# Optimization experiments

Measured on AMD Instinct MI355X. Metric: run time of the kernel, lower is better.

The kernel has to match this reference:

```python
import jax, jax.numpy as jnp
import numpy as np

B = 32768
IN_DIM, OUT_DIM, VAR_DIM = 2, 3, 50
KER_DIMS = [1024, 1024, 1024, 1024]
NSTEPS = 32  # fixed-step RK4 stand-in for adaptive odeint over t in [0, 1]


def setup_inputs() -> dict:
    key = jax.random.key(0)
    ks = jax.random.split(key, 11)
    x = jax.random.normal(ks[0], (B, IN_DIM), dtype=jnp.float32)
    dims = [VAR_DIM] + KER_DIMS + [VAR_DIM]
    inp = {"x": x}
    for i, (d1, d2) in enumerate(zip(dims[:-1], dims[1:])):
        # torch Linear(d1+1, d2): weight (d2, d1+1); stored here as (d1+1, d2)
        bound = 1.0 / np.sqrt(d1 + 1)
        inp[f"W{i}"] = jax.random.uniform(ks[1 + 2 * i], (d1 + 1, d2), jnp.float32, -bound, bound)
        inp[f"b{i}"] = jax.random.uniform(ks[2 + 2 * i], (d2,), jnp.float32, -bound, bound)
    return inp


def _odefunc(t, y, Ws, bs):
    # Each layer: concat time column, Linear, ReLU (except last) -- matches ODEfunc.forward
    out = y
    n = len(Ws)
    for i in range(n):
        tcol = jnp.full((out.shape[0], 1), t, dtype=out.dtype)
        h = jnp.concatenate([out, tcol], axis=1)
        out = h @ Ws[i] + bs[i]
        if i < n - 1:
            out = jax.nn.relu(out)
    return out


def _integrate(x, Ws, bs):
    # Pad input into var_dim state: out[:, :in_dim] = x, rest zeros
    y0 = jnp.zeros((x.shape[0], VAR_DIM), dtype=x.dtype).at[:, : x.shape[1]].set(x)
    dt = jnp.asarray(1.0 / NSTEPS, dtype=x.dtype)
    ts = jnp.arange(NSTEPS, dtype=x.dtype) * dt

    def step(y, t):
        k1 = _odefunc(t, y, Ws, bs)
        k2 = _odefunc(t + dt * 0.5, y + dt * 0.5 * k1, Ws, bs)
        k3 = _odefunc(t + dt * 0.5, y + dt * 0.5 * k2, Ws, bs)
        k4 = _odefunc(t + dt, y + dt * k3, Ws, bs)
        return y + (dt / 6.0) * (k1 + 2.0 * k2 + 2.0 * k3 + k4), None

    y1, _ = jax.lax.scan(step, y0, ts)
    return y1[:, :OUT_DIM]


def reference(x, W0, b0, W1, b1, W2, b2, W3, b3, W4, b4):
    Ws = (W0, W1, W2, W3, W4)
    bs = (b0, b1, b2, b3, b4)
    return _integrate(x, Ws, bs)
```

## Files before the change

kernel.cpp:

```cpp
#include <hip/hip_runtime.h>
#include <hip/hip_bf16.h>
#include <stdint.h>


typedef __bf16 bf16_t;
typedef bf16_t bf16x8 __attribute__((ext_vector_type(8)));
typedef float  f32x4  __attribute__((ext_vector_type(4)));

#define DEVI static __device__ __forceinline__

DEVI void gload_lds16(const bf16_t* gsrc, bf16_t* ldst) {
  __builtin_amdgcn_global_load_lds(
      (const __attribute__((address_space(1))) uint32_t*)gsrc,
      (__attribute__((address_space(3))) uint32_t*)ldst,
      16, 0, 0);
}

template<int K>
__global__ __launch_bounds__(512, 2) void gemm256(
    const bf16_t* __restrict__ A,
    const bf16_t* __restrict__ BT,
    const float* __restrict__ bias,
    const float* __restrict__ wtime,
    float t,
    bf16_t* __restrict__ C, int ldc,
    int M, int N)
{
  constexpr int NT = K / 64;
  static_assert(NT >= 2, "need >=2 K-tiles");

  __shared__ __align__(16) bf16_t As[2][256][64];
  __shared__ __align__(16) bf16_t Bs[2][256][64];

  const int tid  = threadIdx.x;
  const int wave = tid >> 6;
  const int lane = tid & 63;
  const int wr = wave >> 2;
  const int wc = wave & 3;

  int wg = blockIdx.x;
  {
    const int cpx = gridDim.x >> 3;
    wg = (wg & 7) * cpx + (wg >> 3);
  }
  const int nbn = N >> 8;
  const int bm = (wg / nbn) << 8;
  const int bn = (wg % nbn) << 8;

  const int srow = lane >> 3;
  const int scol = ((lane & 7) << 3) ^ ((lane & 32) >> 1) ^ ((wave & 1) << 5);
  const bf16_t* aS = A  + (size_t)(bm + wave * 8 + srow) * K + scol;
  const bf16_t* bS = BT + (size_t)(bn + wave * 8 + srow) * K + scol;
  bf16_t* aD = &As[0][0][0] + wave * 8 * 64;
  bf16_t* bD = &Bs[0][0][0] + wave * 8 * 64;

  auto stageHalf = [&](int kt, int isB, int h) {
    const int buf = kt & 1;
    const bf16_t* src = (isB ? bS : aS) + (size_t)(h * 128) * K + kt * 64;
    bf16_t*       dst = (isB ? bD : aD) + (buf * 256 + h * 128) * 64;
    gload_lds16(src,                 dst);
    gload_lds16(src + (size_t)64 * K, dst + 64 * 64);
  };

  const int fr = lane & 15;
  const int fq = lane >> 4;
  const int rsw = ((fr & 4) << 3) ^ ((fr & 8) << 3);

  bf16x8 af[8];
  bf16x8 bfr[8];
  f32x4  acc[8][4] = {};

  auto lda_frag = [&](int buf, int mh) {
    const char* base = (const char*)&As[buf][0][0];
#pragma unroll
    for (int m = 0; m < 4; ++m)
#pragma unroll
      for (int kk = 0; kk < 2; ++kk) {
        int r  = wr * 128 + (mh * 4 + m) * 16 + fr;
        int cb = (kk * 64 + fq * 16) ^ rsw;
        af[m * 2 + kk] = *(const bf16x8*)(base + r * 128 + cb);
      }
  };
  auto ldb_frag = [&](int buf, int nh) {
    const char* base = (const char*)&Bs[buf][0][0];
#pragma unroll
    for (int n = 0; n < 2; ++n)
#pragma unroll
      for (int kk = 0; kk < 2; ++kk) {
        int r  = wc * 64 + (nh * 2 + n) * 16 + fr;
        int cb = (kk * 64 + fq * 16) ^ rsw;
        bfr[nh * 4 + n * 2 + kk] = *(const bf16x8*)(base + r * 128 + cb);
      }
  };
  auto mma_quad = [&](int mh, int nh) {
    __builtin_amdgcn_s_setprio(1);
#pragma unroll
    for (int m = 0; m < 4; ++m)
#pragma unroll
      for (int n = 0; n < 2; ++n)
#pragma unroll
        for (int kk = 0; kk < 2; ++kk)
          acc[mh * 4 + m][nh * 2 + n] = __builtin_amdgcn_mfma_f32_16x16x32_bf16(
              af[m * 2 + kk], bfr[nh * 4 + n * 2 + kk],
              acc[mh * 4 + m][nh * 2 + n], 0, 0, 0);
    __builtin_amdgcn_s_setprio(0);
  };

  stageHalf(0, 0, 0); stageHalf(0, 1, 0);
  stageHalf(0, 0, 1); stageHalf(0, 1, 1);
  stageHalf(1, 1, 0); stageHalf(1, 0, 0);
  asm volatile("s_waitcnt vmcnt(4)" ::: "memory");
  __builtin_amdgcn_s_barrier();

  for (int t2 = 0; t2 < NT; ++t2) {
    const int buf = t2 & 1;
    lda_frag(buf, 0);
    ldb_frag(buf, 0);
    if (t2 + 1 < NT) stageHalf(t2 + 1, 0, 1);
    __builtin_amdgcn_s_barrier();
    mma_quad(0, 0);
    __builtin_amdgcn_s_barrier();
    ldb_frag(buf, 1);
    if (t2 + 1 < NT) stageHalf(t2 + 1, 1, 1);
    __builtin_amdgcn_s_barrier();
    mma_quad(0, 1);
    __builtin_amdgcn_s_barrier();
    lda_frag(buf, 1);
    if (t2 + 2 < NT) stageHalf(t2 + 2, 1, 0);
    __builtin_amdgcn_s_barrier();
    mma_quad(1, 0);
    __builtin_amdgcn_s_barrier();
    if (t2 + 2 < NT) {
      stageHalf(t2 + 2, 0, 0);
      asm volatile("s_waitcnt vmcnt(4)" ::: "memory");
    } else {
      asm volatile("s_waitcnt vmcnt(0)" ::: "memory");
    }
    __builtin_amdgcn_s_barrier();
    mma_quad(1, 1);
    __builtin_amdgcn_s_barrier();
  }

#pragma unroll
  for (int n = 0; n < 4; ++n) {
    const int gcol = bn + wc * 64 + n * 16 + fr;
    const float bv = bias[gcol] + t * wtime[gcol];
#pragma unroll
    for (int m = 0; m < 8; ++m) {
      const int grow0 = bm + wr * 128 + m * 16 + (fq << 2);
#pragma unroll
      for (int r = 0; r < 4; ++r) {
        float v = acc[m][n][r] + bv;
        v = v > 0.0f ? v : 0.0f;
        C[(size_t)(grow0 + r) * ldc + gcol] = (bf16_t)v;
      }
    }
  }
}

template<int BM, int BN, int BK, int WROWS, int WCOLS, bool RELU, bool OUT_BF16>
__global__ __launch_bounds__(256) void gemm_bt(
    const bf16_t* __restrict__ A, int lda,
    const bf16_t* __restrict__ BT,
    const float* __restrict__ bias,
    const float* __restrict__ wtime,
    float t,
    void* __restrict__ Cv, int ldc,
    int M, int K)
{
  static_assert(BK == 64, "swizzle assumes BK=64");
  constexpr int MR  = BM / WROWS / 16;
  constexpr int NR  = BN / WCOLS / 16;
  constexpr int TPR = BK / 8;
  constexpr int RPW = 64 / TPR;
  constexpr int RPL = 4 * RPW;
  static_assert(BM % RPL == 0 && BN % RPL == 0, "tile staging mismatch");

  __shared__ bf16_t As[BM][BK];
  __shared__ bf16_t Bs[BN][BK];

  const int tid  = threadIdx.x;
  const int wave = tid >> 6;
  const int lane = tid & 63;
  const int wr = wave / WCOLS;
  const int wc = wave % WCOLS;
  const int bm = blockIdx.x * BM;
  const int bn = blockIdx.y * BN;
  const int lrow = lane >> 3;
  const int lcol = (((lane & 7) << 3) ^ ((lane & 32) >> 1) ^ ((wave & 1) << 5));

  const int fr = lane & 15;
  const int fq = lane >> 4;
  const int esw = ((fr & 4) << 2) ^ ((fr & 8) << 2);

  f32x4 acc[MR][NR] = {};

  for (int k0 = 0; k0 < K; k0 += BK) {
#pragma unroll
    for (int i = 0; i < BM / RPL; ++i) {
      const int rb = i * RPL + wave * RPW;
      gload_lds16(&A[(size_t)(bm + rb + lrow) * lda + k0 + lcol], &As[rb][0]);
    }
#pragma unroll
    for (int i = 0; i < BN / RPL; ++i) {
      const int rb = i * RPL + wave * RPW;
      gload_lds16(&BT[(size_t)(bn + rb + lrow) * K + k0 + lcol], &Bs[rb][0]);
    }
    __syncthreads();
#pragma unroll
    for (int kk = 0; kk < BK / 32; ++kk) {
      bf16x8 af[MR], bfr[NR];
      const int ecol = (kk * 32 + fq * 8) ^ esw;
#pragma unroll
      for (int m = 0; m < MR; ++m)
        af[m] = *(const bf16x8*)&As[wr * (BM / WROWS) + m * 16 + fr][ecol];
#pragma unroll
      for (int n = 0; n < NR; ++n)
        bfr[n] = *(const bf16x8*)&Bs[wc * (BN / WCOLS) + n * 16 + fr][ecol];
#pragma unroll
      for (int m = 0; m < MR; ++m)
#pragma unroll
        for (int n = 0; n < NR; ++n)
          acc[m][n] = __builtin_amdgcn_mfma_f32_16x16x32_bf16(
              af[m], bfr[n], acc[m][n], 0, 0, 0);
    }
    __syncthreads();
  }

#pragma unroll
  for (int n = 0; n < NR; ++n) {
    const int gcol = bn + wc * (BN / WCOLS) + n * 16 + fr;
    const float bv = bias[gcol] + t * wtime[gcol];
#pragma unroll
    for (int m = 0; m < MR; ++m) {
      const int grow0 = bm + wr * (BM / WROWS) + m * 16 + (fq << 2);
#pragma unroll
      for (int r = 0; r < 4; ++r) {
        float v = acc[m][n][r] + bv;
        if (RELU) v = v > 0.0f ? v : 0.0f;
        if constexpr (OUT_BF16)
          ((bf16_t*)Cv)[(size_t)(grow0 + r) * ldc + gcol] = (bf16_t)v;
        else
          ((float*)Cv)[(size_t)(grow0 + r) * ldc + gcol] = v;
      }
    }
  }
}

__global__ __launch_bounds__(256) void gemm_l4_rk4(
    const bf16_t* __restrict__ A, int lda,
    const bf16_t* __restrict__ BT,
    const float* __restrict__ bias,
    const float* __restrict__ wtime,
    float t,
    float* __restrict__ y, float* __restrict__ accb,
    bf16_t* __restrict__ ybf,
    float ca, float cs, int mode,
    int M, int K)
{
  constexpr int BM = 64, BN = 64, BK = 64;
  constexpr int MR = 2, NR = 2;

  __shared__ bf16_t As[BM][BK];
  __shared__ bf16_t Bs[BN][BK];

  const int tid  = threadIdx.x;
  const int wave = tid >> 6;
  const int lane = tid & 63;
  const int wr = wave >> 1;
  const int wc = wave & 1;
  const int bm = blockIdx.x * BM;
  const int lrow = lane >> 3;
  const int lcol = (((lane & 7) << 3) ^ ((lane & 32) >> 1) ^ ((wave & 1) << 5));

  const int fr = lane & 15;
  const int fq = lane >> 4;
  const int esw = ((fr & 4) << 2) ^ ((fr & 8) << 2);

  f32x4 acc[MR][NR] = {};

  for (int k0 = 0; k0 < K; k0 += BK) {
#pragma unroll
    for (int i = 0; i < 2; ++i) {
      const int rb = i * 32 + wave * 8;
      gload_lds16(&A[(size_t)(bm + rb + lrow) * lda + k0 + lcol], &As[rb][0]);
    }
#pragma unroll
    for (int i = 0; i < 2; ++i) {
      const int rb = i * 32 + wave * 8;
      gload_lds16(&BT[(size_t)(rb + lrow) * K + k0 + lcol], &Bs[rb][0]);
    }
    __syncthreads();
#pragma unroll
    for (int kk = 0; kk < 2; ++kk) {
      bf16x8 af[MR], bfr[NR];
      const int ecol = (kk * 32 + fq * 8) ^ esw;
#pragma unroll
      for (int m = 0; m < MR; ++m)
        af[m] = *(const bf16x8*)&As[wr * 32 + m * 16 + fr][ecol];
#pragma unroll
      for (int n = 0; n < NR; ++n)
        bfr[n] = *(const bf16x8*)&Bs[wc * 32 + n * 16 + fr][ecol];
#pragma unroll
      for (int m = 0; m < MR; ++m)
#pragma unroll
        for (int n = 0; n < NR; ++n)
          acc[m][n] = __builtin_amdgcn_mfma_f32_16x16x32_bf16(
              af[m], bfr[n], acc[m][n], 0, 0, 0);
    }
    __syncthreads();
  }

#pragma unroll
  for (int n = 0; n < NR; ++n) {
    const int gcol = wc * 32 + n * 16 + fr;
    const float bv = bias[gcol] + t * wtime[gcol];
#pragma unroll
    for (int m = 0; m < MR; ++m) {
      const int grow0 = bm + wr * 32 + m * 16 + (fq << 2);
#pragma unroll
      for (int r = 0; r < 4; ++r) {
        const float kv = acc[m][n][r] + bv;
        const size_t o = (size_t)(grow0 + r) * 64 + gcol;
        if (mode == 0) {
          accb[o] = kv;
          ybf[o] = (bf16_t)(y[o] + cs * kv);
        } else if (mode == 1) {
          accb[o] += ca * kv;
          ybf[o] = (bf16_t)(y[o] + cs * kv);
        } else {
          const float ny = y[o] + cs * (accb[o] + kv);
          y[o] = ny;
          ybf[o] = (bf16_t)ny;
        }
      }
    }
  }
}

__global__ void prep_weight(const float* __restrict__ W, const float* __restrict__ b,
                            bf16_t* __restrict__ WT, float* __restrict__ bias,
                            float* __restrict__ wtime,
                            int K, int N, int Kpad, int Npad)
{
  int idx = blockIdx.x * 256 + threadIdx.x;
  int total = Npad * Kpad;
  if (idx < total) {
    int n = idx / Kpad, k = idx % Kpad;
    float v = (n < N && k < K) ? W[(size_t)k * N + n] : 0.0f;
    WT[idx] = (bf16_t)v;
  }
  if (idx < Npad) {
    bias[idx]  = (idx < N) ? b[idx] : 0.0f;
    wtime[idx] = (idx < N) ? W[(size_t)K * N + idx] : 0.0f;
  }
}

__global__ void init_y(const float* __restrict__ x, float* __restrict__ y,
                       bf16_t* __restrict__ ybf, int M)
{
  int i = blockIdx.x * 256 + threadIdx.x;
  if (i < M * 64) {
    int m = i >> 6, c = i & 63;
    float v = (c < 2) ? x[m * 2 + c] : 0.0f;
    y[i] = v;
    ybf[i] = (bf16_t)v;
  }
}

__global__ void extract_out(const float* __restrict__ y, float* __restrict__ out, int M)
{
  int i = blockIdx.x * 256 + threadIdx.x;
  if (i < M * 3) {
    int m = i / 3, c = i % 3;
    out[i] = y[(size_t)m * 64 + c];
  }
}

extern "C" void kernel_launch(void* const* d_in, const int* in_sizes, int n_in,
                              void* d_out, int out_size, void* d_ws, size_t ws_size,
                              hipStream_t stream)
{
  (void)in_sizes; (void)n_in; (void)out_size; (void)ws_size;
  const int M = 32768;

  const float* x = (const float*)d_in[0];
  const float* Wp[5]; const float* bp[5];
  for (int i = 0; i < 5; ++i) {
    Wp[i] = (const float*)d_in[1 + 2 * i];
    bp[i] = (const float*)d_in[2 + 2 * i];
  }

  char* ws = (char*)d_ws; size_t off = 0;
  auto alloc = [&](size_t bytes) -> char* {
    char* p = ws + off; off += (bytes + 255) & ~(size_t)255; return p;
  };

  bf16_t* WT[5];
  WT[0] = (bf16_t*)alloc((size_t)1024 * 64 * 2);
  WT[1] = (bf16_t*)alloc((size_t)1024 * 1024 * 2);
  WT[2] = (bf16_t*)alloc((size_t)1024 * 1024 * 2);
  WT[3] = (bf16_t*)alloc((size_t)1024 * 1024 * 2);
  WT[4] = (bf16_t*)alloc((size_t)64 * 1024 * 2);
  float* bias[5]; float* wtm[5];
  for (int i = 0; i < 5; ++i) {
    int Np = (i == 4) ? 64 : 1024;
    bias[i] = (float*)alloc((size_t)Np * 4);
    wtm[i]  = (float*)alloc((size_t)Np * 4);
  }
  float*  y    = (float*)alloc((size_t)M * 64 * 4);
  float*  accb = (float*)alloc((size_t)M * 64 * 4);
  bf16_t* ybf  = (bf16_t*)alloc((size_t)M * 64 * 2);
  bf16_t* act0 = (bf16_t*)alloc((size_t)M * 1024 * 2);
  bf16_t* act1 = (bf16_t*)alloc((size_t)M * 1024 * 2);

  const int Kd[5]  = {50, 1024, 1024, 1024, 1024};
  const int Nd[5]  = {1024, 1024, 1024, 1024, 50};
  const int Kpd[5] = {64, 1024, 1024, 1024, 1024};
  const int Npd[5] = {1024, 1024, 1024, 1024, 64};
  for (int i = 0; i < 5; ++i) {
    int tot = Npd[i] * Kpd[i];
    prep_weight<<<dim3((tot + 255) / 256), 256, 0, stream>>>(
        Wp[i], bp[i], WT[i], bias[i], wtm[i], Kd[i], Nd[i], Kpd[i], Npd[i]);
  }

  init_y<<<dim3((M * 64 + 255) / 256), 256, 0, stream>>>(x, y, ybf, M);

  const float dtv = 1.0f / 32.0f;
  dim3 gL0(M / 128, 1024 / 128);
  dim3 g256(M / 256 * (1024 / 256));
  dim3 gL4(M / 64);

  auto run_net = [&](float t, float ca, float cs, int mode) {
    gemm_bt<128,128,64,2,2,true,true><<<gL0, 256, 0, stream>>>(
        ybf, 64, WT[0], bias[0], wtm[0], t, act0, 1024, M, 64);
    gemm256<1024><<<g256, 512, 0, stream>>>(
        act0, WT[1], bias[1], wtm[1], t, act1, 1024, M, 1024);
    gemm256<1024><<<g256, 512, 0, stream>>>(
        act1, WT[2], bias[2], wtm[2], t, act0, 1024, M, 1024);
    gemm256<1024><<<g256, 512, 0, stream>>>(
        act0, WT[3], bias[3], wtm[3], t, act1, 1024, M, 1024);
    gemm_l4_rk4<<<gL4, 256, 0, stream>>>(
        act1, 1024, WT[4], bias[4], wtm[4], t,
        y, accb, ybf, ca, cs, mode, M, 1024);
  };

  for (int i = 0; i < 32; ++i) {
    const float t0 = i * dtv;
    const float tm = t0 + 0.5f * dtv;
    const float t1 = t0 + dtv;
    run_net(t0, 0.0f, 0.5f * dtv, 0);
    run_net(tm, 2.0f, 0.5f * dtv, 1);
    run_net(tm, 2.0f, dtv,        1);
    run_net(t1, 0.0f, dtv / 6.0f, 2);
  }

  extract_out<<<dim3((M * 3 + 255) / 256), 256, 0, stream>>>(y, (float*)d_out, M);
}
```

Before: 39.33 ms.

## Restructure GEMM main loop with whole-tile prefetch and register double-buffered fragments

The four-quadrant K-loop used eight barriers per iteration and staged half-tiles two steps ahead. It is replaced by a schedule that prefetches the entire next K-tile into the other LDS buffer at the top of each iteration. A/B fragments are split into two register sets so the next tile's first fragments load while the last quadrant's MFMAs run, with only one barrier per iteration. The intent is to cut barrier stalls and overlap LDS reads with matrix math. The cost is more live fragment registers under the 512x2 launch bound, and a full vmcnt(0) wait each iteration that may expose global-load latency.

```diff
diff --git a/kernel.cpp b/kernel.cpp
--- a/kernel.cpp
+++ b/kernel.cpp
@@ -58,19 +58,23 @@
     const int buf = kt & 1;
     const bf16_t* src = (isB ? bS : aS) + (size_t)(h * 128) * K + kt * 64;
     bf16_t*       dst = (isB ? bD : aD) + (buf * 256 + h * 128) * 64;
-    gload_lds16(src,                 dst);
+    gload_lds16(src,                  dst);
     gload_lds16(src + (size_t)64 * K, dst + 64 * 64);
+  };
+  auto stageTile = [&](int kt) {
+    stageHalf(kt, 0, 0); stageHalf(kt, 0, 1);
+    stageHalf(kt, 1, 0); stageHalf(kt, 1, 1);
   };
 
   const int fr = lane & 15;
   const int fq = lane >> 4;
   const int rsw = ((fr & 4) << 3) ^ ((fr & 8) << 3);
 
-  bf16x8 af[8];
-  bf16x8 bfr[8];
+  bf16x8 ah0[8], ah1[8];
+  bf16x8 bh0[4], bh1[4];
   f32x4  acc[8][4] = {};
 
-  auto lda_frag = [&](int buf, int mh) {
+  auto lda_into = [&](bf16x8 (&dst)[8], int buf, int mh) {
     const char* base = (const char*)&As[buf][0][0];
 #pragma unroll
     for (int m = 0; m < 4; ++m)
@@ -78,10 +82,10 @@
       for (int kk = 0; kk < 2; ++kk) {
         int r  = wr * 128 + (mh * 4 + m) * 16 + fr;
         int cb = (kk * 64 + fq * 16) ^ rsw;
-        af[m * 2 + kk] = *(const bf16x8*)(base + r * 128 + cb);
+        dst[m * 2 + kk] = *(const bf16x8*)(base + r * 128 + cb);
       }
   };
-  auto ldb_frag = [&](int buf, int nh) {
+  auto ldb_into = [&](bf16x8 (&dst)[4], int buf, int nh) {
     const char* base = (const char*)&Bs[buf][0][0];
 #pragma unroll
     for (int n = 0; n < 2; ++n)
@@ -89,10 +93,10 @@
       for (int kk = 0; kk < 2; ++kk) {
         int r  = wc * 64 + (nh * 2 + n) * 16 + fr;
         int cb = (kk * 64 + fq * 16) ^ rsw;
-        bfr[nh * 4 + n * 2 + kk] = *(const bf16x8*)(base + r * 128 + cb);
+        dst[n * 2 + kk] = *(const bf16x8*)(base + r * 128 + cb);
       }
   };
-  auto mma_quad = [&](int mh, int nh) {
+  auto mma_quad = [&](bf16x8 (&a)[8], bf16x8 (&b)[4], int mh, int nh) {
     __builtin_amdgcn_s_setprio(1);
 #pragma unroll
     for (int m = 0; m < 4; ++m)
@@ -101,44 +105,32 @@
 #pragma unroll
         for (int kk = 0; kk < 2; ++kk)
           acc[mh * 4 + m][nh * 2 + n] = __builtin_amdgcn_mfma_f32_16x16x32_bf16(
-              af[m * 2 + kk], bfr[nh * 4 + n * 2 + kk],
+              a[m * 2 + kk], b[n * 2 + kk],
               acc[mh * 4 + m][nh * 2 + n], 0, 0, 0);
     __builtin_amdgcn_s_setprio(0);
   };
 
-  stageHalf(0, 0, 0); stageHalf(0, 1, 0);
-  stageHalf(0, 0, 1); stageHalf(0, 1, 1);
-  stageHalf(1, 1, 0); stageHalf(1, 0, 0);
-  asm volatile("s_waitcnt vmcnt(4)" ::: "memory");
+  stageTile(0);
+  asm volatile("s_waitcnt vmcnt(0)" ::: "memory");
   __builtin_amdgcn_s_barrier();
+  lda_into(ah0, 0, 0);
+  ldb_into(bh0, 0, 0);
 
   for (int t2 = 0; t2 < NT; ++t2) {
     const int buf = t2 & 1;
-    lda_frag(buf, 0);
-    ldb_frag(buf, 0);
-    if (t2 + 1 < NT) stageHalf(t2 + 1, 0, 1);
-    __builtin_amdgcn_s_barrier();
-    mma_quad(0, 0);
-    __builtin_amdgcn_s_barrier();
-    ldb_frag(buf, 1);
-    if (t2 + 1 < NT) stageHalf(t2 + 1, 1, 1);
-    __builtin_amdgcn_s_barrier();
-    mma_quad(0, 1);
-    __builtin_amdgcn_s_barrier();
-    lda_frag(buf, 1);
-    if (t2 + 2 < NT) stageHalf(t2 + 2, 1, 0);
-    __builtin_amdgcn_s_barrier();
-    mma_quad(1, 0);
-    __builtin_amdgcn_s_barrier();
-    if (t2 + 2 < NT) {
-      stageHalf(t2 + 2, 0, 0);
-      asm volatile("s_waitcnt vmcnt(4)" ::: "memory");
-    } else {
+    if (t2 + 1 < NT) stageTile(t2 + 1);
+    ldb_into(bh1, buf, 1);
+    mma_quad(ah0, bh0, 0, 0);
+    lda_into(ah1, buf, 1);
+    mma_quad(ah0, bh1, 0, 1);
+    mma_quad(ah1, bh0, 1, 0);
+    if (t2 + 1 < NT) {
       asm volatile("s_waitcnt vmcnt(0)" ::: "memory");
-    }
-    __builtin_amdgcn_s_barrier();
-    mma_quad(1, 1);
-    __builtin_amdgcn_s_barrier();
+      __builtin_amdgcn_s_barrier();
+      lda_into(ah0, buf ^ 1, 0);
+      ldb_into(bh0, buf ^ 1, 0);
+    }
+    mma_quad(ah1, bh1, 1, 1);
   }
 
 #pragma unroll
```

Result: faster. 35.17 ms (-10.6%).
